# Kernel optimization log

Hardware: AMD Instinct MI355X
Metric: run time of the kernel (lower is better)

The kernel has to match this reference:

```python
import jax, jax.numpy as jnp
import numpy as np

N, D, H = 4096, 1024, 8
DH = D // H
EPS = 1e-5


def layer_norm(x, g, b):
    mu = jnp.mean(x, axis=-1, keepdims=True)
    var = jnp.mean(jnp.square(x - mu), axis=-1, keepdims=True)
    return (x - mu) * jax.lax.rsqrt(var + EPS) * g + b


def setup_inputs() -> dict:
    key = jax.random.key(0)
    ks = jax.random.split(key, 12)
    s = 0.02
    inp = {
        "x": jax.random.normal(ks[0], (N, D), dtype=jnp.float32),
        "adj": (jax.random.uniform(ks[1], (N, N)) < 0.01).astype(jnp.float32),
        "Wq": jax.random.normal(ks[2], (D, D), dtype=jnp.float32) * s,
        "Wk": jax.random.normal(ks[3], (D, D), dtype=jnp.float32) * s,
        "Wv": jax.random.normal(ks[4], (D, D), dtype=jnp.float32) * s,
        "Wo_w": jax.random.normal(ks[5], (D, D), dtype=jnp.float32) * s,
        "Wo_b": jnp.zeros((D,), dtype=jnp.float32),
        "adj_bias": jnp.full((H,), 1.0, dtype=jnp.float32),
        "ln1_g": jnp.ones((D,), dtype=jnp.float32),
        "ln1_b": jnp.zeros((D,), dtype=jnp.float32),
        "ffn_ln_g": jnp.ones((D,), dtype=jnp.float32),
        "ffn_ln_b": jnp.zeros((D,), dtype=jnp.float32),
        "ffn_w1": jax.random.normal(ks[6], (D, 2 * D), dtype=jnp.float32) * s,
        "ffn_b1": jnp.zeros((2 * D,), dtype=jnp.float32),
        "ffn_w2": jax.random.normal(ks[7], (2 * D, D), dtype=jnp.float32) * s,
        "ffn_b2": jnp.zeros((D,), dtype=jnp.float32),
    }
    return inp


def reference(x, adj, Wq, Wk, Wv, Wo_w, Wo_b, adj_bias, ln1_g, ln1_b,
              ffn_ln_g, ffn_ln_b, ffn_w1, ffn_b1, ffn_w2, ffn_b2):
    scale = DH ** -0.5
    Q = (x @ Wq).reshape(N, H, DH)
    K = (x @ Wk).reshape(N, H, DH)
    V = (x @ Wv).reshape(N, H, DH)
    # attn[i,h,j] = <Q_i, K_j> * scale + beta_h * adj[i,j]
    attn = jnp.einsum('bhd,nhd->bhn', Q, K) * scale
    attn = attn + adj_bias[None, :, None] * adj[:, None, :]
    attn = jax.nn.softmax(attn, axis=-1)  # dropout in eval mode -> identity
    out = jnp.einsum('bhn,nhd->bhd', attn, V).reshape(N, D)
    out = out @ Wo_w + Wo_b
    h = layer_norm(x + out, ln1_g, ln1_b)
    f = layer_norm(h, ffn_ln_g, ffn_ln_b)
    f = jax.nn.gelu(f @ ffn_w1 + ffn_b1, approximate=False) @ ffn_w2 + ffn_b2
    return h + f
```

## Files before the change

kernel.cpp:

```cpp
#include <hip/hip_runtime.h>
#include <hip/hip_bf16.h>
#include <cstdint>
#include <cstddef>

typedef __hip_bfloat16 bf16;
typedef __attribute__((ext_vector_type(8))) short short8;
typedef __attribute__((ext_vector_type(4))) short short4v;
typedef __attribute__((ext_vector_type(4))) float floatx4;
typedef unsigned long long u64;

#define DEVI static __device__ __forceinline__

DEVI void load_lds16(const void* g, void* l) {
  __builtin_amdgcn_global_load_lds((const __attribute__((address_space(1))) unsigned int*)g,
                                   (__attribute__((address_space(3))) unsigned int*)l, 16, 0, 0);
}
DEVI short8 ld8(const bf16* p) { return *(const short8*)p; }
DEVI floatx4 mfma16(short8 a, short8 b, floatx4 c) {
  return __builtin_amdgcn_mfma_f32_16x16x32_bf16(a, b, c, 0, 0, 0);
}
DEVI short bfb(float f) { bf16 h = __float2bfloat16(f); return __builtin_bit_cast(short, h); }
DEVI float fbf(short s) { bf16 h = __builtin_bit_cast(bf16, s); return __bfloat162float(h); }

__global__ __launch_bounds__(256) void cvt_kernel(const float* __restrict__ in,
                                                  bf16* __restrict__ out, int n4) {
  int i = blockIdx.x * 256 + threadIdx.x;
  if (i < n4) {
    float4 v = ((const float4*)in)[i];
    bf16* o = out + (size_t)i * 4;
    o[0] = __float2bfloat16(v.x); o[1] = __float2bfloat16(v.y);
    o[2] = __float2bfloat16(v.z); o[3] = __float2bfloat16(v.w);
  }
}

DEVI void tr_body(const float* in, bf16* out, int R, int C) {
  __shared__ float t[32][33];
  int c0 = blockIdx.x * 32, r0 = blockIdx.y * 32;
  int tx = threadIdx.x, ty = threadIdx.y;
#pragma unroll
  for (int i = 0; i < 32; i += 8) t[ty + i][tx] = in[(size_t)(r0 + ty + i) * C + c0 + tx];
  __syncthreads();
#pragma unroll
  for (int i = 0; i < 32; i += 8)
    out[(size_t)(c0 + ty + i) * R + r0 + tx] = __float2bfloat16(t[tx][ty + i]);
}

__global__ __launch_bounds__(256) void tr_f32_bf16(const float* __restrict__ in,
                                                   bf16* __restrict__ out, int R, int C) {
  tr_body(in, out, R, C);
}

__global__ __launch_bounds__(256)
void tr_f32_bf16_4(const float* i0, const float* i1, const float* i2, const float* i3,
                   bf16* o0, bf16* o1, bf16* o2, bf16* o3) {
  const float* in = blockIdx.z == 0 ? i0 : blockIdx.z == 1 ? i1 : blockIdx.z == 2 ? i2 : i3;
  bf16* out = blockIdx.z == 0 ? o0 : blockIdx.z == 1 ? o1 : blockIdx.z == 2 ? o2 : o3;
  tr_body(in, out, 1024, 1024);
}

__global__ __launch_bounds__(256)
void tr_bf16p(const bf16* __restrict__ in, bf16* __restrict__ out, int inLd) {
  __shared__ bf16 t[32][33];
  int c0 = blockIdx.x * 32, r0 = blockIdx.y * 32;
  int tx = threadIdx.x, ty = threadIdx.y;
#pragma unroll
  for (int i = 0; i < 32; i += 8) t[ty + i][tx] = in[(size_t)(r0 + ty + i) * inLd + c0 + tx];
  __syncthreads();
#pragma unroll
  for (int i = 0; i < 32; i += 8) {
    int k = r0 + tx;
    int pk = (k & ~63) | ((k & 15) << 2) | ((k >> 4) & 3);
    out[(size_t)(c0 + ty + i) * 4096 + pk] = t[tx][ty + i];
  }
}

__global__ __launch_bounds__(256)
void adjbits_kernel(const float* __restrict__ adj, u64* __restrict__ bits) {
  int row = blockIdx.x, tid = threadIdx.x;
  int wave = tid >> 6, lane = tid & 63;
  const float* arow = adj + (size_t)row * 4096;
#pragma unroll
  for (int it = 0; it < 16; it++) {
    int col = it * 256 + tid;
    u64 m = __ballot(arow[col] != 0.f);
    if (lane == 0) bits[(size_t)row * 64 + it * 4 + wave] = m;
  }
}

template <int MODE>
__global__ __launch_bounds__(256)
void gemm_bt(const bf16* __restrict__ A, const bf16* __restrict__ Bt,
             const float* __restrict__ bias, const float* __restrict__ resid,
             float* __restrict__ outF, bf16* __restrict__ outB,
             int M, int Nn, int K) {
  __shared__ alignas(16) bf16 As[128 * 32];
  __shared__ alignas(16) bf16 Bs[128 * 32];
  const int tid = threadIdx.x;
  const int wave = tid >> 6, lane = tid & 63;
  const int m0 = blockIdx.y * 128, n0 = blockIdx.x * 128;
  const int wr = (wave >> 1) * 64, wc = (wave & 1) * 64;
  const int l15 = lane & 15, qq = lane >> 4;
  const int lr = lane >> 2, l4 = lane & 3;

  floatx4 acc[4][4];
#pragma unroll
  for (int i = 0; i < 4; i++)
#pragma unroll
    for (int j = 0; j < 4; j++) acc[i][j] = (floatx4)0.f;

  const bf16* gA0 = A + (size_t)(m0 + wave * 16 + lr) * K + l4 * 8;
  const bf16* gA1 = gA0 + (size_t)64 * K;
  const bf16* gB0 = Bt + (size_t)(n0 + wave * 16 + lr) * K + l4 * 8;
  const bf16* gB1 = gB0 + (size_t)64 * K;
  bf16* lA0 = As + wave * 16 * 32;
  bf16* lA1 = As + (64 + wave * 16) * 32;
  bf16* lB0 = Bs + wave * 16 * 32;
  bf16* lB1 = Bs + (64 + wave * 16) * 32;

  for (int kt = 0; kt < K; kt += 32) {
    __syncthreads();
    load_lds16(gA0 + kt, lA0);
    load_lds16(gA1 + kt, lA1);
    load_lds16(gB0 + kt, lB0);
    load_lds16(gB1 + kt, lB1);
    asm volatile("s_waitcnt vmcnt(0)" ::: "memory");
    __syncthreads();
    short8 af[4], bfr[4];
#pragma unroll
    for (int mi = 0; mi < 4; mi++) af[mi] = ld8(&As[(wr + mi * 16 + l15) * 32 + qq * 8]);
#pragma unroll
    for (int ni = 0; ni < 4; ni++) bfr[ni] = ld8(&Bs[(wc + ni * 16 + l15) * 32 + qq * 8]);
#pragma unroll
    for (int mi = 0; mi < 4; mi++)
#pragma unroll
      for (int ni = 0; ni < 4; ni++)
        acc[mi][ni] = mfma16(af[mi], bfr[ni], acc[mi][ni]);
  }

#pragma unroll
  for (int mi = 0; mi < 4; mi++) {
    int row = m0 + wr + mi * 16 + qq * 4;
#pragma unroll
    for (int ni = 0; ni < 4; ni++) {
      int col = n0 + wc + ni * 16 + l15;
      float bv = (MODE >= 1) ? bias[col] : 0.f;
#pragma unroll
      for (int r = 0; r < 4; r++) {
        float v = acc[mi][ni][r] + bv;
        size_t off = (size_t)(row + r) * Nn + col;
        if (MODE == 0) {
          outB[off] = __float2bfloat16(v);
        } else if (MODE == 1) {
          outF[off] = v;
        } else if (MODE == 2) {
          outB[off] = __float2bfloat16(0.5f * v * (1.f + erff(v * 0.70710678118654752f)));
        } else {
          outF[off] = v + resid[off];
        }
      }
    }
  }
}

__global__ __launch_bounds__(256, 2)
void attn_kernel(const bf16* __restrict__ QKV, const bf16* __restrict__ Vtp,
                 const u64* __restrict__ adjbits, const float* __restrict__ adj_bias,
                 bf16* __restrict__ AOpart, float* __restrict__ lpart) {
  __shared__ alignas(16) bf16 Kf[16 * 512];
  __shared__ alignas(16) bf16 Vf[16 * 512];
  __shared__ alignas(16) bf16 Ps[4][32 * 68];
  __shared__ u64 Abits[128 * 16];
  const int q0 = blockIdx.x * 128;
  const int h = blockIdx.y;
  const int split = blockIdx.z;
  const int k0 = split * 1024;
  const int tid = threadIdx.x, wave = tid >> 6, lane = tid & 63;
  const int l15 = lane & 15, qq = lane >> 4;
  const float beta = adj_bias[h];
  const float scale = 0.08838834764831845f;

#pragma unroll
  for (int i = 0; i < 8; i++) {
    int idx = tid + i * 256;
    Abits[idx] = adjbits[(size_t)(q0 + (idx >> 4)) * 64 + split * 16 + (idx & 15)];
  }

  short8 qf[2][4];
#pragma unroll
  for (int mi = 0; mi < 2; mi++)
#pragma unroll
    for (int kk = 0; kk < 4; kk++)
      qf[mi][kk] = ld8(&QKV[(size_t)(q0 + wave * 32 + mi * 16 + l15) * 3072 +
                            h * 128 + kk * 32 + qq * 8]);

  floatx4 o[2][8];
#pragma unroll
  for (int mi = 0; mi < 2; mi++)
#pragma unroll
    for (int ni = 0; ni < 8; ni++) o[mi][ni] = (floatx4)0.f;
  float lrow[2][4];
#pragma unroll
  for (int mi = 0; mi < 2; mi++)
#pragma unroll
    for (int r = 0; r < 4; r++) lrow[mi][r] = 0.f;

  bf16* PsW = &Ps[wave][0];

  short8 kpre[4], vpre[4];
  auto fetchK = [&](int kt, short8* dst) {
#pragma unroll
    for (int i = 0; i < 4; i++) {
      int fi = wave * 4 + i, ni = fi >> 2, kk = fi & 3;
      dst[i] = ld8(&QKV[(size_t)(kt + ni * 16 + l15) * 3072 + 1024 +
                        h * 128 + kk * 32 + qq * 8]);
    }
  };
  auto fetchV = [&](int kt, short8* dst) {
#pragma unroll
    for (int i = 0; i < 4; i++) {
      int fi = wave * 4 + i, ni = fi >> 1, kk = fi & 1;
      dst[i] = ld8(&Vtp[(size_t)(h * 128 + ni * 16 + l15) * 4096 + kt + kk * 32 + qq * 8]);
    }
  };
  fetchK(k0, kpre);
  fetchV(k0, vpre);

  for (int t = 0; t < 16; t++) {
    const int kt = k0 + t * 64;
    __syncthreads();
#pragma unroll
    for (int i = 0; i < 4; i++) {
      *(short8*)&Kf[(wave * 4 + i) * 512 + lane * 8] = kpre[i];
      *(short8*)&Vf[(wave * 4 + i) * 512 + lane * 8] = vpre[i];
    }
    __syncthreads();
    if (t < 15) { fetchK(kt + 64, kpre); fetchV(kt + 64, vpre); }

#pragma unroll
    for (int mi = 0; mi < 2; mi++) {
      floatx4 s[4];
#pragma unroll
      for (int ni = 0; ni < 4; ni++) s[ni] = (floatx4)0.f;
#pragma unroll
      for (int kk = 0; kk < 4; kk++) {
#pragma unroll
        for (int ni = 0; ni < 4; ni++) {
          short8 kf = ld8(&Kf[(ni * 4 + kk) * 512 + lane * 8]);
          s[ni] = mfma16(qf[mi][kk], kf, s[ni]);
        }
      }
#pragma unroll
      for (int r = 0; r < 4; r++) {
        int rloc = wave * 32 + mi * 16 + qq * 4 + r;
        u64 bits = Abits[rloc * 16 + t];
        unsigned lo = (unsigned)(bits >> l15);
        unsigned hi = (unsigned)(bits >> (l15 + 32));
        float b0 = (lo & 1u) ? beta : 0.f;
        float b1 = (lo & 0x10000u) ? beta : 0.f;
        float b2 = (hi & 1u) ? beta : 0.f;
        float b3 = (hi & 0x10000u) ? beta : 0.f;
        float p0 = __expf(fmaf(s[0][r], scale, b0));
        float p1 = __expf(fmaf(s[1][r], scale, b1));
        float p2 = __expf(fmaf(s[2][r], scale, b2));
        float p3 = __expf(fmaf(s[3][r], scale, b3));
        lrow[mi][r] += (p0 + p1) + (p2 + p3);
        short4v pk;
        pk.x = bfb(p0); pk.y = bfb(p1); pk.z = bfb(p2); pk.w = bfb(p3);
        *(short4v*)&PsW[(mi * 16 + qq * 4 + r) * 68 + l15 * 4] = pk;
      }
    }

#pragma unroll
    for (int kk = 0; kk < 2; kk++) {
      short8 af0 = ld8(&PsW[(0 + l15) * 68 + kk * 32 + qq * 8]);
      short8 af1 = ld8(&PsW[(16 + l15) * 68 + kk * 32 + qq * 8]);
#pragma unroll
      for (int ni = 0; ni < 8; ni++) {
        short8 vf = ld8(&Vf[(ni * 2 + kk) * 512 + lane * 8]);
        o[0][ni] = mfma16(af0, vf, o[0][ni]);
        o[1][ni] = mfma16(af1, vf, o[1][ni]);
      }
    }
  }

#pragma unroll
  for (int mi = 0; mi < 2; mi++) {
#pragma unroll
    for (int r = 0; r < 4; r++) {
      float v = lrow[mi][r];
#pragma unroll
      for (int ofs = 1; ofs < 16; ofs <<= 1) v += __shfl_xor(v, ofs, 16);
      int rloc = wave * 32 + mi * 16 + qq * 4 + r;
      int grow = q0 + rloc;
      if (l15 == 0) lpart[((size_t)split * 4096 + grow) * 8 + h] = v;
      bf16* dst = AOpart + ((size_t)split * 4096 + grow) * 1024 + h * 128;
#pragma unroll
      for (int ni = 0; ni < 8; ni++) dst[ni * 16 + l15] = __float2bfloat16(o[mi][ni][r]);
    }
  }
}

__global__ __launch_bounds__(256)
void attn_norm(const bf16* __restrict__ AOpart, const float* __restrict__ lpart,
               bf16* __restrict__ AO) {
  int row = blockIdx.x, tid = threadIdx.x;
  int h = tid >> 5;
  float ls = 0.f;
#pragma unroll
  for (int s = 0; s < 4; s++) ls += lpart[((size_t)s * 4096 + row) * 8 + h];
  float a0 = 0.f, a1 = 0.f, a2 = 0.f, a3 = 0.f;
#pragma unroll
  for (int s = 0; s < 4; s++) {
    short4v v = *(const short4v*)&AOpart[((size_t)s * 4096 + row) * 1024 + tid * 4];
    a0 += fbf(v.x); a1 += fbf(v.y); a2 += fbf(v.z); a3 += fbf(v.w);
  }
  float inv = 1.f / ls;
  bf16* op = AO + (size_t)row * 1024 + tid * 4;
  op[0] = __float2bfloat16(a0 * inv);
  op[1] = __float2bfloat16(a1 * inv);
  op[2] = __float2bfloat16(a2 * inv);
  op[3] = __float2bfloat16(a3 * inv);
}

DEVI void block_sum2(float& a, float& b, float* red) {
#pragma unroll
  for (int o = 1; o < 64; o <<= 1) { a += __shfl_xor(a, o, 64); b += __shfl_xor(b, o, 64); }
  int wv = threadIdx.x >> 6;
  if ((threadIdx.x & 63) == 0) { red[wv] = a; red[4 + wv] = b; }
  __syncthreads();
  a = red[0] + red[1] + red[2] + red[3];
  b = red[4] + red[5] + red[6] + red[7];
  __syncthreads();
}

__global__ __launch_bounds__(256)
void ln2_kernel(const float* __restrict__ x, const float* __restrict__ ao,
                const float* __restrict__ g1, const float* __restrict__ b1,
                const float* __restrict__ g2, const float* __restrict__ b2,
                float* __restrict__ hout, bf16* __restrict__ fln) {
  __shared__ float red[8];
  const int row = blockIdx.x, tid = threadIdx.x;
  float4 xv = ((const float4*)(x + (size_t)row * 1024))[tid];
  float4 av = ((const float4*)(ao + (size_t)row * 1024))[tid];
  float s0 = xv.x + av.x, s1 = xv.y + av.y, s2 = xv.z + av.z, s3 = xv.w + av.w;
  float sum = s0 + s1 + s2 + s3;
  float ssq = s0 * s0 + s1 * s1 + s2 * s2 + s3 * s3;
  block_sum2(sum, ssq, red);
  float mu = sum * (1.f / 1024.f);
  float rs = rsqrtf(ssq * (1.f / 1024.f) - mu * mu + 1e-5f);
  float4 gv = ((const float4*)g1)[tid], bv = ((const float4*)b1)[tid];
  float h0 = (s0 - mu) * rs * gv.x + bv.x;
  float h1 = (s1 - mu) * rs * gv.y + bv.y;
  float h2 = (s2 - mu) * rs * gv.z + bv.z;
  float h3 = (s3 - mu) * rs * gv.w + bv.w;
  float4 hv; hv.x = h0; hv.y = h1; hv.z = h2; hv.w = h3;
  ((float4*)(hout + (size_t)row * 1024))[tid] = hv;
  float sum2 = h0 + h1 + h2 + h3;
  float ssq2 = h0 * h0 + h1 * h1 + h2 * h2 + h3 * h3;
  block_sum2(sum2, ssq2, red);
  float mu2 = sum2 * (1.f / 1024.f);
  float rs2 = rsqrtf(ssq2 * (1.f / 1024.f) - mu2 * mu2 + 1e-5f);
  float4 g2v = ((const float4*)g2)[tid], b2v = ((const float4*)b2)[tid];
  bf16* op = fln + (size_t)row * 1024 + tid * 4;
  op[0] = __float2bfloat16((h0 - mu2) * rs2 * g2v.x + b2v.x);
  op[1] = __float2bfloat16((h1 - mu2) * rs2 * g2v.y + b2v.y);
  op[2] = __float2bfloat16((h2 - mu2) * rs2 * g2v.z + b2v.z);
  op[3] = __float2bfloat16((h3 - mu2) * rs2 * g2v.w + b2v.w);
}

extern "C" void kernel_launch(void* const* d_in, const int* in_sizes, int n_in,
                              void* d_out, int out_size, void* d_ws, size_t ws_size,
                              hipStream_t stream) {
  const float* x    = (const float*)d_in[0];
  const float* adj  = (const float*)d_in[1];
  const float* Wq   = (const float*)d_in[2];
  const float* Wk   = (const float*)d_in[3];
  const float* Wv   = (const float*)d_in[4];
  const float* Wo   = (const float*)d_in[5];
  const float* Wob  = (const float*)d_in[6];
  const float* adjb = (const float*)d_in[7];
  const float* g1   = (const float*)d_in[8];
  const float* b1   = (const float*)d_in[9];
  const float* g2   = (const float*)d_in[10];
  const float* b2   = (const float*)d_in[11];
  const float* W1   = (const float*)d_in[12];
  const float* fb1  = (const float*)d_in[13];
  const float* W2   = (const float*)d_in[14];
  const float* fb2  = (const float*)d_in[15];
  float* out = (float*)d_out;

  char* w = (char*)d_ws;
  size_t off = 0;
  auto take = [&](size_t bytes) {
    char* p = w + off;
    off += (bytes + 255) & ~(size_t)255;
    return p;
  };
  bf16* xb    = (bf16*)take(4096ull * 1024 * 2);
  bf16* Wqkvt = (bf16*)take(3072ull * 1024 * 2);
  bf16* Wot   = (bf16*)take(1024ull * 1024 * 2);
  bf16* W1t   = (bf16*)take(2048ull * 1024 * 2);
  bf16* W2t   = (bf16*)take(1024ull * 2048 * 2);
  bf16* QKV   = (bf16*)take(4096ull * 3072 * 2);
  bf16* Vtp   = (bf16*)take(1024ull * 4096 * 2);
  bf16* AO    = (bf16*)take(4096ull * 1024 * 2);
  u64*  adjbits = (u64*)take(4096ull * 64 * 8);
  float* lpart  = (float*)take(4ull * 4096 * 8 * 4);
  char* big = take(64ull << 20);
  bf16*  AOpart = (bf16*)big;
  float* AOP = (float*)big;
  float* H   = (float*)(big + (16ull << 20));
  bf16*  FLN = (bf16*)(big + (32ull << 20));
  bf16*  G   = (bf16*)(big + (40ull << 20));

  dim3 tb(32, 8);
  cvt_kernel<<<4096, 256, 0, stream>>>(x, xb, 1048576);
  adjbits_kernel<<<4096, 256, 0, stream>>>(adj, adjbits);
  tr_f32_bf16_4<<<dim3(32, 32, 4), tb, 0, stream>>>(
      Wq, Wk, Wv, Wo, Wqkvt, Wqkvt + 1024ull * 1024, Wqkvt + 2048ull * 1024, Wot);
  tr_f32_bf16<<<dim3(64, 32), tb, 0, stream>>>(W1, W1t, 1024, 2048);
  tr_f32_bf16<<<dim3(32, 64), tb, 0, stream>>>(W2, W2t, 2048, 1024);

  gemm_bt<0><<<dim3(24, 32), 256, 0, stream>>>(xb, Wqkvt, nullptr, nullptr, nullptr, QKV,
                                               4096, 3072, 1024);
  tr_bf16p<<<dim3(32, 128), tb, 0, stream>>>(QKV + 2048, Vtp, 3072);
  attn_kernel<<<dim3(32, 8, 4), 256, 0, stream>>>(QKV, Vtp, adjbits, adjb, AOpart, lpart);
  attn_norm<<<4096, 256, 0, stream>>>(AOpart, lpart, AO);
  gemm_bt<1><<<dim3(8, 32), 256, 0, stream>>>(AO, Wot, Wob, nullptr, AOP, nullptr,
                                              4096, 1024, 1024);
  ln2_kernel<<<4096, 256, 0, stream>>>(x, AOP, g1, b1, g2, b2, H, FLN);
  gemm_bt<2><<<dim3(16, 32), 256, 0, stream>>>(FLN, W1t, fb1, nullptr, nullptr, G,
                                               4096, 2048, 1024);
  gemm_bt<3><<<dim3(8, 32), 256, 0, stream>>>(G, W2t, fb2, H, out, nullptr,
                                              4096, 1024, 2048);
}
```

Measured before the change: 469.2 us.

## Pipeline GEMM loads with triple buffering, split-K small GEMMs, merge prep kernels

The GEMM main loop now uses a three-stage LDS ring filled by async global-to-LDS loads, which replaces the fully synchronous load/wait/compute step. The two N=1024 GEMMs are split along K into two partial outputs that ln2 or a new add kernel sums, so more blocks are in flight. The prep kernels (convert, adjacency bits, all weight transposes) are merged into fewer launches. The attention kernel reads adjacency bits straight into registers with prefetch instead of staging them in LDS, and its occupancy bound is raised to 3. Split-K adds extra float partial traffic and an extra add pass, and the higher occupancy bound may cause register spills.

```diff
diff --git a/kernel.cpp b/kernel.cpp
--- a/kernel.cpp
+++ b/kernel.cpp
@@ -22,20 +22,27 @@
 DEVI short bfb(float f) { bf16 h = __float2bfloat16(f); return __builtin_bit_cast(short, h); }
 DEVI float fbf(short s) { bf16 h = __builtin_bit_cast(bf16, s); return __bfloat162float(h); }
 
-__global__ __launch_bounds__(256) void cvt_kernel(const float* __restrict__ in,
-                                                  bf16* __restrict__ out, int n4) {
-  int i = blockIdx.x * 256 + threadIdx.x;
-  if (i < n4) {
-    float4 v = ((const float4*)in)[i];
-    bf16* o = out + (size_t)i * 4;
-    o[0] = __float2bfloat16(v.x); o[1] = __float2bfloat16(v.y);
-    o[2] = __float2bfloat16(v.z); o[3] = __float2bfloat16(v.w);
-  }
-}
-
-DEVI void tr_body(const float* in, bf16* out, int R, int C) {
+__global__ __launch_bounds__(256)
+void prep_kernel(const float* __restrict__ x, bf16* __restrict__ xb,
+                 const float* __restrict__ adj, u64* __restrict__ bits) {
+  const int row = blockIdx.x, tid = threadIdx.x;
+  const int wave = tid >> 6, lane = tid & 63;
+  float4 v = ((const float4*)(x + (size_t)row * 1024))[tid];
+  bf16* o = xb + (size_t)row * 1024 + tid * 4;
+  o[0] = __float2bfloat16(v.x); o[1] = __float2bfloat16(v.y);
+  o[2] = __float2bfloat16(v.z); o[3] = __float2bfloat16(v.w);
+  const float* arow = adj + (size_t)row * 4096;
+#pragma unroll
+  for (int it = 0; it < 16; it++) {
+    int col = it * 256 + tid;
+    u64 m = __ballot(arow[col] != 0.f);
+    if (lane == 0) bits[(size_t)row * 64 + it * 4 + wave] = m;
+  }
+}
+
+DEVI void tr_tile(const float* in, bf16* out, int R, int C, int bx, int by) {
   __shared__ float t[32][33];
-  int c0 = blockIdx.x * 32, r0 = blockIdx.y * 32;
+  int c0 = bx * 32, r0 = by * 32;
   int tx = threadIdx.x, ty = threadIdx.y;
 #pragma unroll
   for (int i = 0; i < 32; i += 8) t[ty + i][tx] = in[(size_t)(r0 + ty + i) * C + c0 + tx];
@@ -45,17 +52,24 @@
     out[(size_t)(c0 + ty + i) * R + r0 + tx] = __float2bfloat16(t[tx][ty + i]);
 }
 
-__global__ __launch_bounds__(256) void tr_f32_bf16(const float* __restrict__ in,
-                                                   bf16* __restrict__ out, int R, int C) {
-  tr_body(in, out, R, C);
-}
-
-__global__ __launch_bounds__(256)
-void tr_f32_bf16_4(const float* i0, const float* i1, const float* i2, const float* i3,
-                   bf16* o0, bf16* o1, bf16* o2, bf16* o3) {
-  const float* in = blockIdx.z == 0 ? i0 : blockIdx.z == 1 ? i1 : blockIdx.z == 2 ? i2 : i3;
-  bf16* out = blockIdx.z == 0 ? o0 : blockIdx.z == 1 ? o1 : blockIdx.z == 2 ? o2 : o3;
-  tr_body(in, out, 1024, 1024);
+__global__ __launch_bounds__(256)
+void tr_all(const float* Wq, const float* Wk, const float* Wv, const float* Wo,
+            const float* W1, const float* W2,
+            bf16* Wqkvt, bf16* Wot, bf16* W1t, bf16* W2t) {
+  int id = blockIdx.x;
+  if (id < 4096) {
+    int w = id >> 10, t = id & 1023;
+    const float* in = w == 0 ? Wq : w == 1 ? Wk : w == 2 ? Wv : Wo;
+    bf16* out = w == 0 ? Wqkvt : w == 1 ? Wqkvt + 1024ull * 1024
+                : w == 2 ? Wqkvt + 2048ull * 1024 : Wot;
+    tr_tile(in, out, 1024, 1024, t & 31, t >> 5);
+  } else if (id < 6144) {
+    int t = id - 4096;
+    tr_tile(W1, W1t, 1024, 2048, t & 63, t >> 6);
+  } else {
+    int t = id - 6144;
+    tr_tile(W2, W2t, 2048, 1024, t & 31, t >> 5);
+  }
 }
 
 __global__ __launch_bounds__(256)
@@ -74,33 +88,23 @@
   }
 }
 
-__global__ __launch_bounds__(256)
-void adjbits_kernel(const float* __restrict__ adj, u64* __restrict__ bits) {
-  int row = blockIdx.x, tid = threadIdx.x;
-  int wave = tid >> 6, lane = tid & 63;
-  const float* arow = adj + (size_t)row * 4096;
-#pragma unroll
-  for (int it = 0; it < 16; it++) {
-    int col = it * 256 + tid;
-    u64 m = __ballot(arow[col] != 0.f);
-    if (lane == 0) bits[(size_t)row * 64 + it * 4 + wave] = m;
-  }
-}
-
 template <int MODE>
 __global__ __launch_bounds__(256)
 void gemm_bt(const bf16* __restrict__ A, const bf16* __restrict__ Bt,
              const float* __restrict__ bias, const float* __restrict__ resid,
              float* __restrict__ outF, bf16* __restrict__ outB,
              int M, int Nn, int K) {
-  __shared__ alignas(16) bf16 As[128 * 32];
-  __shared__ alignas(16) bf16 Bs[128 * 32];
+  __shared__ alignas(16) bf16 As[3][128 * 32];
+  __shared__ alignas(16) bf16 Bs[3][128 * 32];
   const int tid = threadIdx.x;
   const int wave = tid >> 6, lane = tid & 63;
   const int m0 = blockIdx.y * 128, n0 = blockIdx.x * 128;
   const int wr = (wave >> 1) * 64, wc = (wave & 1) * 64;
   const int l15 = lane & 15, qq = lane >> 4;
   const int lr = lane >> 2, l4 = lane & 3;
+  const int Kspan = K / gridDim.z;
+  const int kbeg = blockIdx.z * Kspan;
+  const int T = Kspan >> 5;
 
   floatx4 acc[4][4];
 #pragma unroll
@@ -108,68 +112,76 @@
 #pragma unroll
     for (int j = 0; j < 4; j++) acc[i][j] = (floatx4)0.f;
 
-  const bf16* gA0 = A + (size_t)(m0 + wave * 16 + lr) * K + l4 * 8;
+  const bf16* gA0 = A + (size_t)(m0 + wave * 16 + lr) * K + kbeg + l4 * 8;
   const bf16* gA1 = gA0 + (size_t)64 * K;
-  const bf16* gB0 = Bt + (size_t)(n0 + wave * 16 + lr) * K + l4 * 8;
+  const bf16* gB0 = Bt + (size_t)(n0 + wave * 16 + lr) * K + kbeg + l4 * 8;
   const bf16* gB1 = gB0 + (size_t)64 * K;
-  bf16* lA0 = As + wave * 16 * 32;
-  bf16* lA1 = As + (64 + wave * 16) * 32;
-  bf16* lB0 = Bs + wave * 16 * 32;
-  bf16* lB1 = Bs + (64 + wave * 16) * 32;
-
-  for (int kt = 0; kt < K; kt += 32) {
-    __syncthreads();
-    load_lds16(gA0 + kt, lA0);
-    load_lds16(gA1 + kt, lA1);
-    load_lds16(gB0 + kt, lB0);
-    load_lds16(gB1 + kt, lB1);
-    asm volatile("s_waitcnt vmcnt(0)" ::: "memory");
-    __syncthreads();
+  const int lo = wave * 16 * 32;
+
+  auto stage = [&](int t, int buf) {
+    int kt = t * 32;
+    load_lds16(gA0 + kt, &As[buf][lo]);
+    load_lds16(gA1 + kt, &As[buf][64 * 32 + lo]);
+    load_lds16(gB0 + kt, &Bs[buf][lo]);
+    load_lds16(gB1 + kt, &Bs[buf][64 * 32 + lo]);
+  };
+  stage(0, 0);
+  stage(1, 1);
+
+  int bc = 0;
+  for (int t = 0; t < T; ++t) {
+    if (t < T - 1) asm volatile("s_waitcnt vmcnt(4) lgkmcnt(0)" ::: "memory");
+    else           asm volatile("s_waitcnt vmcnt(0) lgkmcnt(0)" ::: "memory");
+    __builtin_amdgcn_s_barrier();
+    if (t + 2 < T) { int bs = bc == 0 ? 2 : bc - 1; stage(t + 2, bs); }
+
     short8 af[4], bfr[4];
 #pragma unroll
-    for (int mi = 0; mi < 4; mi++) af[mi] = ld8(&As[(wr + mi * 16 + l15) * 32 + qq * 8]);
-#pragma unroll
-    for (int ni = 0; ni < 4; ni++) bfr[ni] = ld8(&Bs[(wc + ni * 16 + l15) * 32 + qq * 8]);
+    for (int mi = 0; mi < 4; mi++) af[mi] = ld8(&As[bc][(wr + mi * 16 + l15) * 32 + qq * 8]);
+#pragma unroll
+    for (int ni = 0; ni < 4; ni++) bfr[ni] = ld8(&Bs[bc][(wc + ni * 16 + l15) * 32 + qq * 8]);
 #pragma unroll
     for (int mi = 0; mi < 4; mi++)
 #pragma unroll
       for (int ni = 0; ni < 4; ni++)
         acc[mi][ni] = mfma16(af[mi], bfr[ni], acc[mi][ni]);
-  }
-
+    bc = bc == 2 ? 0 : bc + 1;
+  }
+
+  const size_t zoff = (size_t)blockIdx.z * M * Nn;
 #pragma unroll
   for (int mi = 0; mi < 4; mi++) {
     int row = m0 + wr + mi * 16 + qq * 4;
 #pragma unroll
     for (int ni = 0; ni < 4; ni++) {
       int col = n0 + wc + ni * 16 + l15;
-      float bv = (MODE >= 1) ? bias[col] : 0.f;
+      float bv = 0.f;
+      if (MODE == 2) bv = bias[col];
+      if (MODE == 4 && blockIdx.z == 0) bv = bias[col];
 #pragma unroll
       for (int r = 0; r < 4; r++) {
         float v = acc[mi][ni][r] + bv;
         size_t off = (size_t)(row + r) * Nn + col;
         if (MODE == 0) {
           outB[off] = __float2bfloat16(v);
-        } else if (MODE == 1) {
-          outF[off] = v;
         } else if (MODE == 2) {
           outB[off] = __float2bfloat16(0.5f * v * (1.f + erff(v * 0.70710678118654752f)));
         } else {
-          outF[off] = v + resid[off];
+          if (resid && blockIdx.z == 1) v += resid[off];
+          outF[zoff + off] = v;
         }
       }
     }
   }
 }
 
-__global__ __launch_bounds__(256, 2)
+__global__ __launch_bounds__(256, 3)
 void attn_kernel(const bf16* __restrict__ QKV, const bf16* __restrict__ Vtp,
                  const u64* __restrict__ adjbits, const float* __restrict__ adj_bias,
                  bf16* __restrict__ AOpart, float* __restrict__ lpart) {
   __shared__ alignas(16) bf16 Kf[16 * 512];
   __shared__ alignas(16) bf16 Vf[16 * 512];
   __shared__ alignas(16) bf16 Ps[4][32 * 68];
-  __shared__ u64 Abits[128 * 16];
   const int q0 = blockIdx.x * 128;
   const int h = blockIdx.y;
   const int split = blockIdx.z;
@@ -179,12 +191,6 @@
   const float beta = adj_bias[h];
   const float scale = 0.08838834764831845f;
 
-#pragma unroll
-  for (int i = 0; i < 8; i++) {
-    int idx = tid + i * 256;
-    Abits[idx] = adjbits[(size_t)(q0 + (idx >> 4)) * 64 + split * 16 + (idx & 15)];
-  }
-
   short8 qf[2][4];
 #pragma unroll
   for (int mi = 0; mi < 2; mi++)
@@ -207,6 +213,7 @@
   bf16* PsW = &Ps[wave][0];
 
   short8 kpre[4], vpre[4];
+  u64 abc[2][4], abn[2][4];
   auto fetchK = [&](int kt, short8* dst) {
 #pragma unroll
     for (int i = 0; i < 4; i++) {
@@ -222,8 +229,17 @@
       dst[i] = ld8(&Vtp[(size_t)(h * 128 + ni * 16 + l15) * 4096 + kt + kk * 32 + qq * 8]);
     }
   };
+  auto fetchA = [&](int t, u64 (*ab)[4]) {
+#pragma unroll
+    for (int mi = 0; mi < 2; mi++)
+#pragma unroll
+      for (int r = 0; r < 4; r++)
+        ab[mi][r] = adjbits[(size_t)(q0 + wave * 32 + mi * 16 + qq * 4 + r) * 64 +
+                            split * 16 + t];
+  };
   fetchK(k0, kpre);
   fetchV(k0, vpre);
+  fetchA(0, abc);
 
   for (int t = 0; t < 16; t++) {
     const int kt = k0 + t * 64;
@@ -234,7 +250,7 @@
       *(short8*)&Vf[(wave * 4 + i) * 512 + lane * 8] = vpre[i];
     }
     __syncthreads();
-    if (t < 15) { fetchK(kt + 64, kpre); fetchV(kt + 64, vpre); }
+    if (t < 15) { fetchK(kt + 64, kpre); fetchV(kt + 64, vpre); fetchA(t + 1, abn); }
 
 #pragma unroll
     for (int mi = 0; mi < 2; mi++) {
@@ -251,8 +267,7 @@
       }
 #pragma unroll
       for (int r = 0; r < 4; r++) {
-        int rloc = wave * 32 + mi * 16 + qq * 4 + r;
-        u64 bits = Abits[rloc * 16 + t];
+        u64 bits = abc[mi][r];
         unsigned lo = (unsigned)(bits >> l15);
         unsigned hi = (unsigned)(bits >> (l15 + 32));
         float b0 = (lo & 1u) ? beta : 0.f;
@@ -281,6 +296,10 @@
         o[1][ni] = mfma16(af1, vf, o[1][ni]);
       }
     }
+#pragma unroll
+    for (int mi = 0; mi < 2; mi++)
+#pragma unroll
+      for (int r = 0; r < 4; r++) abc[mi][r] = abn[mi][r];
   }
 
 #pragma unroll
@@ -334,15 +353,18 @@
 }
 
 __global__ __launch_bounds__(256)
-void ln2_kernel(const float* __restrict__ x, const float* __restrict__ ao,
+void ln2_kernel(const float* __restrict__ x, const float* __restrict__ ao0,
+                const float* __restrict__ ao1,
                 const float* __restrict__ g1, const float* __restrict__ b1,
                 const float* __restrict__ g2, const float* __restrict__ b2,
                 float* __restrict__ hout, bf16* __restrict__ fln) {
   __shared__ float red[8];
   const int row = blockIdx.x, tid = threadIdx.x;
   float4 xv = ((const float4*)(x + (size_t)row * 1024))[tid];
-  float4 av = ((const float4*)(ao + (size_t)row * 1024))[tid];
-  float s0 = xv.x + av.x, s1 = xv.y + av.y, s2 = xv.z + av.z, s3 = xv.w + av.w;
+  float4 av = ((const float4*)(ao0 + (size_t)row * 1024))[tid];
+  float4 aw = ((const float4*)(ao1 + (size_t)row * 1024))[tid];
+  float s0 = xv.x + av.x + aw.x, s1 = xv.y + av.y + aw.y;
+  float s2 = xv.z + av.z + aw.z, s3 = xv.w + av.w + aw.w;
   float sum = s0 + s1 + s2 + s3;
   float ssq = s0 * s0 + s1 * s1 + s2 * s2 + s3 * s3;
   block_sum2(sum, ssq, red);
@@ -368,6 +390,17 @@
   op[3] = __float2bfloat16((h3 - mu2) * rs2 * g2v.w + b2v.w);
 }
 
+__global__ __launch_bounds__(256)
+void add2_kernel(const float* __restrict__ a, const float* __restrict__ b,
+                 float* __restrict__ o) {
+  int i = blockIdx.x * 256 + threadIdx.x;
+  float4 va = ((const float4*)a)[i];
+  float4 vb = ((const float4*)b)[i];
+  float4 vo; vo.x = va.x + vb.x; vo.y = va.y + vb.y;
+  vo.z = va.z + vb.z; vo.w = va.w + vb.w;
+  ((float4*)o)[i] = vo;
+}
+
 extern "C" void kernel_launch(void* const* d_in, const int* in_sizes, int n_in,
                               void* d_out, int out_size, void* d_ws, size_t ws_size,
                               hipStream_t stream) {
@@ -406,31 +439,29 @@
   bf16* AO    = (bf16*)take(4096ull * 1024 * 2);
   u64*  adjbits = (u64*)take(4096ull * 64 * 8);
   float* lpart  = (float*)take(4ull * 4096 * 8 * 4);
-  char* big = take(64ull << 20);
+  char* big = take(32ull << 20);
   bf16*  AOpart = (bf16*)big;
-  float* AOP = (float*)big;
-  float* H   = (float*)(big + (16ull << 20));
-  bf16*  FLN = (bf16*)(big + (32ull << 20));
-  bf16*  G   = (bf16*)(big + (40ull << 20));
+  float* WoP    = (float*)big;
+  float* F2P    = (float*)big;
+  float* H   = (float*)take(4096ull * 1024 * 4);
+  bf16*  FLN = (bf16*)take(4096ull * 1024 * 2);
+  bf16*  G   = (bf16*)take(4096ull * 2048 * 2);
 
   dim3 tb(32, 8);
-  cvt_kernel<<<4096, 256, 0, stream>>>(x, xb, 1048576);
-  adjbits_kernel<<<4096, 256, 0, stream>>>(adj, adjbits);
-  tr_f32_bf16_4<<<dim3(32, 32, 4), tb, 0, stream>>>(
-      Wq, Wk, Wv, Wo, Wqkvt, Wqkvt + 1024ull * 1024, Wqkvt + 2048ull * 1024, Wot);
-  tr_f32_bf16<<<dim3(64, 32), tb, 0, stream>>>(W1, W1t, 1024, 2048);
-  tr_f32_bf16<<<dim3(32, 64), tb, 0, stream>>>(W2, W2t, 2048, 1024);
-
-  gemm_bt<0><<<dim3(24, 32), 256, 0, stream>>>(xb, Wqkvt, nullptr, nullptr, nullptr, QKV,
-                                               4096, 3072, 1024);
+  prep_kernel<<<4096, 256, 0, stream>>>(x, xb, adj, adjbits);
+  tr_all<<<8192, tb, 0, stream>>>(Wq, Wk, Wv, Wo, W1, W2, Wqkvt, Wot, W1t, W2t);
+
+  gemm_bt<0><<<dim3(24, 32, 1), 256, 0, stream>>>(xb, Wqkvt, nullptr, nullptr,
+                                                  nullptr, QKV, 4096, 3072, 1024);
   tr_bf16p<<<dim3(32, 128), tb, 0, stream>>>(QKV + 2048, Vtp, 3072);
   attn_kernel<<<dim3(32, 8, 4), 256, 0, stream>>>(QKV, Vtp, adjbits, adjb, AOpart, lpart);
   attn_norm<<<4096, 256, 0, stream>>>(AOpart, lpart, AO);
-  gemm_bt<1><<<dim3(8, 32), 256, 0, stream>>>(AO, Wot, Wob, nullptr, AOP, nullptr,
-                                              4096, 1024, 1024);
-  ln2_kernel<<<4096, 256, 0, stream>>>(x, AOP, g1, b1, g2, b2, H, FLN);
-  gemm_bt<2><<<dim3(16, 32), 256, 0, stream>>>(FLN, W1t, fb1, nullptr, nullptr, G,
-                                               4096, 2048, 1024);
-  gemm_bt<3><<<dim3(8, 32), 256, 0, stream>>>(G, W2t, fb2, H, out, nullptr,
-                                              4096, 1024, 2048);
-}
+  gemm_bt<4><<<dim3(8, 32, 2), 256, 0, stream>>>(AO, Wot, Wob, nullptr,
+                                                 WoP, nullptr, 4096, 1024, 1024);
+  ln2_kernel<<<4096, 256, 0, stream>>>(x, WoP, WoP + 4096ull * 1024, g1, b1, g2, b2, H, FLN);
+  gemm_bt<2><<<dim3(16, 32, 1), 256, 0, stream>>>(FLN, W1t, fb1, nullptr,
+                                                  nullptr, G, 4096, 2048, 1024);
+  gemm_bt<4><<<dim3(8, 32, 2), 256, 0, stream>>>(G, W2t, fb2, H,
+                                                 F2P, nullptr, 4096, 1024, 2048);
+  add2_kernel<<<4096, 256, 0, stream>>>(F2P, F2P + 4096ull * 1024, out);
+}
```

After: 491.2 us. +4.7%, slower.
